# Performance work log

Hardware: AMD Instinct MI355X
Metric: run time of the kernel (lower is better)

The kernel has to match this reference:

```python
import jax, jax.numpy as jnp
import numpy as np

B, N, D, H, DH = 2, 2048, 1024, 16, 64
SCALE = DH ** -0.5


def rotate_half(t):
    t1, t2 = jnp.split(t, 2, axis=-1)
    return jnp.concatenate([-t2, t1], axis=-1)


def setup_inputs() -> dict:
    key = jax.random.key(0)
    ks = jax.random.split(key, 10)
    x = jax.random.normal(ks[0], (B, N, D), jnp.float32)
    mask = jnp.ones((B, N), bool)
    rotary_emb = jax.random.normal(ks[1], (N, DH), jnp.float32)
    attn_bias = jax.random.normal(ks[2], (H, N, N), jnp.float32)
    value_residual = jax.random.normal(ks[3], (B, H, N, DH), jnp.float32)
    s = D ** -0.5
    Wq = jax.random.normal(ks[4], (D, H * DH), jnp.float32) * s
    Wkv = jax.random.normal(ks[5], (D, 2 * H * DH), jnp.float32) * s
    Wmix = jax.random.normal(ks[6], (D, H), jnp.float32) * s
    Wout = jax.random.normal(ks[7], (H * DH, D), jnp.float32) * s
    bout = jnp.zeros((D,), jnp.float32)
    return {"x": x, "mask": mask, "rotary_emb": rotary_emb, "attn_bias": attn_bias,
            "value_residual": value_residual, "Wq": Wq, "Wkv": Wkv, "Wmix": Wmix,
            "Wout": Wout, "bout": bout}


def reference(x, mask, rotary_emb, attn_bias, value_residual, Wq, Wkv, Wmix, Wout, bout):
    b, n, _ = x.shape
    # QKV projections (self-attention: context = x)
    q = (x @ Wq).reshape(b, n, H, DH).transpose(0, 2, 1, 3)          # b h n d
    kv = (x @ Wkv).reshape(b, n, 2, H, DH).transpose(2, 0, 3, 1, 4)
    k, v = kv[0], kv[1]                                              # b h n d each
    # value-residual lerp: v.lerp(residual, mix) = v + mix*(residual - v)
    mix = jax.nn.sigmoid(x @ Wmix).transpose(0, 2, 1)[..., None]     # b h n 1
    v = v + mix * (value_residual - v)
    # rotary position embedding on q and k
    cos = jnp.cos(rotary_emb)[None, None]                            # 1 1 n d
    sin = jnp.sin(rotary_emb)[None, None]
    q = q * cos + rotate_half(q) * sin
    k = k * cos + rotate_half(k) * sin
    # scaled dot-product attention with bias and key-padding mask
    sim = jnp.einsum('bhid,bhjd->bhij', q, k) * SCALE + attn_bias[None]
    neg = jnp.finfo(sim.dtype).min
    sim = jnp.where(mask[:, None, None, :], sim, neg)
    attn = jax.nn.softmax(sim, axis=-1)
    out = jnp.einsum('bhij,bhjd->bhid', attn, v)
    out = out.transpose(0, 2, 1, 3).reshape(b, n, H * DH)
    return out @ Wout + bout
```

## Files before the change

kernel.cpp:

```cpp
#include <hip/hip_runtime.h>
#include <hip/hip_bf16.h>
#include <cstdint>
#include <cstddef>

#define B_    2
#define N_    2048
#define D_    1024
#define H_    16
#define DH_   64
#define HD_   1024
#define QKVW_ 3072
#define SCALE_ 0.125f

typedef unsigned short ushort_t;
typedef __attribute__((ext_vector_type(8))) short bf16x8;
typedef __attribute__((ext_vector_type(4))) float f32x4;
typedef _Float16 f16_t;
typedef __attribute__((ext_vector_type(8))) _Float16 f16x8;

__device__ __forceinline__ float bfb(unsigned v) {
  union { unsigned u; float f; } c; c.u = v << 16; return c.f;
}
__device__ __forceinline__ float bf2f(ushort_t v) { return bfb((unsigned)v); }
__device__ __forceinline__ ushort_t f2bf(float f) {
  unsigned u = __float_as_uint(f);
  return (ushort_t)((u + 0x7fffu + ((u >> 16) & 1u)) >> 16);
}
__device__ __forceinline__ ushort_t f2h_bits(float f) {
  union { f16_t h; ushort_t u; } c; c.h = (f16_t)f; return c.u;
}

template<bool F32>
__device__ __forceinline__ float ld1(const void* p, size_t i) {
  if (F32) return ((const float*)p)[i];
  else     return bf2f(((const ushort_t*)p)[i]);
}
template<bool F32>
__device__ __forceinline__ void ld4(const void* p, size_t i, float* o) {
  if (F32) {
    float4 v = *(const float4*)((const float*)p + i);
    o[0] = v.x; o[1] = v.y; o[2] = v.z; o[3] = v.w;
  } else {
    ushort4 v = *(const ushort4*)((const ushort_t*)p + i);
    o[0] = bf2f(v.x); o[1] = bf2f(v.y); o[2] = bf2f(v.z); o[3] = bf2f(v.w);
  }
}

__global__ __launch_bounds__(256) void detect_kernel(const unsigned* __restrict__ xbits,
                                                     int* __restrict__ flag) {
  __shared__ int cnt[256];
  int tid = threadIdx.x, bad = 0;
  for (int i = tid; i < 4096; i += 256) {
    unsigned w = xbits[i];
    bad += (((w >> 7) & 0xffu) >= 0xF0u) + (((w >> 23) & 0xffu) >= 0xF0u);
  }
  cnt[tid] = bad;
  __syncthreads();
  for (int s = 128; s > 0; s >>= 1) {
    if (tid < s) cnt[tid] += cnt[tid + s];
    __syncthreads();
  }
  if (tid == 0) *flag = (cnt[0] > 4) ? 1 : 0;
}

template<bool F32>
__global__ __launch_bounds__(64) void mix_kernel(const int* __restrict__ flag,
                                                 const void* __restrict__ x,
                                                 const void* __restrict__ Wmix,
                                                 float* __restrict__ mix) {
  if ((*flag == 1) != F32) return;
  int row  = blockIdx.x;
  int lane = threadIdx.x;
  int h = lane >> 2, part = lane & 3;
  float acc = 0.f;
  int kbase = part * 256;
  for (int t = 0; t < 256; ++t) {
    int k = kbase + t;
    acc = fmaf(ld1<F32>(x, (size_t)row * D_ + k), ld1<F32>(Wmix, (size_t)k * H_ + h), acc);
  }
  acc += __shfl_xor(acc, 1);
  acc += __shfl_xor(acc, 2);
  if (part == 0) mix[(size_t)row * H_ + h] = 1.f / (1.f + __expf(-acc));
}

template<bool F32>
__global__ __launch_bounds__(256) void gemm_qkv_mfma(const int* __restrict__ flag,
                                                     const void* __restrict__ X,
                                                     const void* __restrict__ Wq,
                                                     const void* __restrict__ Wkv,
                                                     ushort_t* __restrict__ C) {
  if ((*flag == 1) != F32) return;
  __shared__ ushort_t As[128 * 40];
  __shared__ ushort_t Bs[128 * 40];
  int tid  = threadIdx.x;
  int w    = tid >> 6, lane = tid & 63;
  int ln   = lane & 15, quad = lane >> 4;
  int wr   = w >> 1, wc = w & 1;
  int n0   = blockIdx.x * 128, m0 = blockIdx.y * 128;
  const void* Bp; int ldb, nb;
  if (n0 < 1024) { Bp = Wq;  ldb = 1024; nb = n0; }
  else           { Bp = Wkv; ldb = 2048; nb = n0 - 1024; }

  f32x4 acc[4][4] = {};

  for (int kt = 0; kt < 32; ++kt) {
    int k0 = kt * 32;
#pragma unroll
    for (int i = 0; i < 2; ++i) {
      int f   = tid + 256 * i;
      int row = f >> 2, c8 = (f & 3) << 3;
      float at[8];
      ld4<F32>(X, (size_t)(m0 + row) * D_ + k0 + c8,     at);
      ld4<F32>(X, (size_t)(m0 + row) * D_ + k0 + c8 + 4, at + 4);
      union { ushort_t s[8]; uint4 u; } hh;
#pragma unroll
      for (int j = 0; j < 8; ++j) hh.s[j] = f2h_bits(at[j]);
      *(uint4*)&As[row * 40 + c8] = hh.u;
    }
#pragma unroll
    for (int i = 0; i < 2; ++i) {
      int p  = tid + 256 * i;
      int kp = p >> 5, c4 = (p & 31) << 2;
      float b0[4], b1[4];
      ld4<F32>(Bp, (size_t)(k0 + 2 * kp)     * ldb + nb + c4, b0);
      ld4<F32>(Bp, (size_t)(k0 + 2 * kp + 1) * ldb + nb + c4, b1);
#pragma unroll
      for (int j = 0; j < 4; ++j) {
        int n  = c4 + j;
        int kk = (2 * kp) ^ (((n >> 2) & 7) << 2);
        *(unsigned*)&Bs[n * 40 + kk] =
            (unsigned)f2h_bits(b0[j]) | ((unsigned)f2h_bits(b1[j]) << 16);
      }
    }
    __syncthreads();
    f16x8 af[4];
#pragma unroll
    for (int i = 0; i < 4; ++i)
      af[i] = *(const f16x8*)&As[(wr * 64 + i * 16 + ln) * 40 + quad * 8];
#pragma unroll
    for (int jb = 0; jb < 4; ++jb) {
      int n = wc * 64 + jb * 16 + ln;
      int ps = ((n >> 2) & 7) << 2;
      union { ushort4 q[2]; f16x8 v; } bf;
      bf.q[0] = *(const ushort4*)&Bs[n * 40 + ((quad * 8)     ^ ps)];
      bf.q[1] = *(const ushort4*)&Bs[n * 40 + ((quad * 8 + 4) ^ ps)];
#pragma unroll
      for (int i = 0; i < 4; ++i)
        acc[i][jb] = __builtin_amdgcn_mfma_f32_16x16x32_f16(af[i], bf.v, acc[i][jb], 0, 0, 0);
    }
    __syncthreads();
  }
#pragma unroll
  for (int i = 0; i < 4; ++i) {
    int row = m0 + wr * 64 + i * 16 + quad * 4;
#pragma unroll
    for (int jb = 0; jb < 4; ++jb) {
      int col = n0 + wc * 64 + jb * 16 + ln;
#pragma unroll
      for (int r = 0; r < 4; ++r)
        C[(size_t)(row + r) * QKVW_ + col] = f2bf(acc[i][jb][r]);
    }
  }
}

template<bool F32>
__global__ __launch_bounds__(256) void rotlerp(const int* __restrict__ flag,
                                               ushort_t* __restrict__ qkv,
                                               const void* __restrict__ rot,
                                               const float* __restrict__ mix,
                                               const void* __restrict__ resid) {
  if ((*flag == 1) != F32) return;
  int lane = threadIdx.x & 63;
  int row  = blockIdx.x * 4 + (threadIdx.x >> 6);
  int h  = row & 15;
  int bn = row >> 4;
  int n  = bn & (N_ - 1);
  int b  = bn >> 11;
  size_t base = (size_t)bn * QKVW_ + h * DH_;
  float q = bf2f(qkv[base + lane]);
  float k = bf2f(qkv[base + 1024 + lane]);
  float v = bf2f(qkv[base + 2048 + lane]);
  float ang = ld1<F32>(rot, (size_t)n * DH_ + lane);
  float sn, cs;
  __sincosf(ang, &sn, &cs);
  float qp = __shfl_xor(q, 32);
  float kp = __shfl_xor(k, 32);
  float sgn = (lane < 32) ? -1.f : 1.f;
  float qn = fmaf(q, cs, sgn * qp * sn);
  float kn = fmaf(k, cs, sgn * kp * sn);
  float m = mix[(size_t)bn * H_ + h];
  float r = ld1<F32>(resid, ((size_t)(b * H_ + h) * N_ + n) * DH_ + lane);
  float vn = fmaf(m, r - v, v);
  qkv[base + lane]        = f2bf(qn);
  qkv[base + 1024 + lane] = f2bf(kn);
  qkv[base + 2048 + lane] = f2bf(vn);
}

template<bool F32>
__global__ __launch_bounds__(256) void attn_mfma(const int* __restrict__ flag,
                                                 const ushort_t* __restrict__ qkv,
                                                 const void* __restrict__ bias,
                                                 ushort_t* __restrict__ obuf) {
  if ((*flag == 1) != F32) return;
  __shared__ ushort_t Ks[64 * 72];
  __shared__ ushort_t Vt[64 * 72];
  __shared__ ushort_t Ps[4][16 * 72];
  int tid  = threadIdx.x;
  int w    = tid >> 6, lane = tid & 63;
  int ln   = lane & 15, quad = lane >> 4;
  int q0   = blockIdx.x * 64, h = blockIdx.y, b = blockIdx.z;

  bf16x8 aq0, aq1;
  {
    const ushort_t* qp = qkv + (size_t)(b * N_ + q0 + 16 * w + ln) * QKVW_ + h * DH_ + quad * 8;
    union { uint4 u; bf16x8 v; } c0, c1;
    c0.u = *(const uint4*)qp;
    c1.u = *(const uint4*)(qp + 32);
    aq0 = c0.v; aq1 = c1.v;
  }
  bf16x8 one_b;
  {
    union { ushort_t s[8]; bf16x8 v; } ob;
#pragma unroll
    for (int i = 0; i < 8; ++i) ob.s[i] = (ln == 0) ? (ushort_t)0x3F80 : (ushort_t)0;
    one_b = ob.v;
  }

  f32x4 o[5] = {};
  float mrow[4] = {-1e30f, -1e30f, -1e30f, -1e30f};

  int rA = tid >> 3;
  int cc = tid & 7;
  int dd = cc * 8;
  uint4 kA, kB, vA, vB;
  float bbA[4][4], bbB[4][4];

  auto loadKV = [&](int t) {
    int j0 = t * 64;
    const ushort_t* kp = qkv + (size_t)(b * N_ + j0 + rA) * QKVW_ + 1024 + h * DH_ + dd;
    kA = *(const uint4*)kp;
    vA = *(const uint4*)(kp + 1024);
    kB = *(const uint4*)(kp + (size_t)32 * QKVW_);
    vB = *(const uint4*)(kp + (size_t)32 * QKVW_ + 1024);
  };
  auto writeKV = [&]() {
    *(uint4*)&Ks[rA * 72 + dd]        = kA;
    *(uint4*)&Ks[(rA + 32) * 72 + dd] = kB;
    union { uint4 u; ushort_t s[8]; } ua, ub;
    ua.u = vA; ub.u = vB;
    int colA = (rA + 8 * cc) & 63;
    int colB = (rA + 32 + 8 * cc) & 63;
#pragma unroll
    for (int i = 0; i < 8; ++i) {
      Vt[(dd + i) * 72 + colA] = ua.s[i];
      Vt[(dd + i) * 72 + colB] = ub.s[i];
    }
  };
  auto loadBias = [&](int t, float (&bb)[4][4]) {
    int j0 = t * 64;
    size_t rbase = (size_t)h * N_ + q0 + 16 * w + quad * 4;
#pragma unroll
    for (int r = 0; r < 4; ++r)
#pragma unroll
      for (int c = 0; c < 4; ++c)
        bb[r][c] = ld1<F32>(bias, (rbase + r) * N_ + j0 + 16 * c + ln);
  };
  auto tileCompute = [&](const float (&bb)[4][4]) {
    f32x4 s[4] = {};
#pragma unroll
    for (int jb = 0; jb < 4; ++jb) {
      bf16x8 k0 = *(const bf16x8*)&Ks[(jb * 16 + ln) * 72 + quad * 8];
      bf16x8 k1 = *(const bf16x8*)&Ks[(jb * 16 + ln) * 72 + 32 + quad * 8];
      s[jb] = __builtin_amdgcn_mfma_f32_16x16x32_bf16(aq0, k0, s[jb], 0, 0, 0);
      s[jb] = __builtin_amdgcn_mfma_f32_16x16x32_bf16(aq1, k1, s[jb], 0, 0, 0);
    }
    float vv[4][4], tm[4];
    float g = -1e30f;
#pragma unroll
    for (int r = 0; r < 4; ++r) {
#pragma unroll
      for (int c = 0; c < 4; ++c) vv[r][c] = fmaf(s[c][r], SCALE_, bb[r][c]);
      float t01 = fmaxf(vv[r][0], vv[r][1]);
      float t23 = fmaxf(vv[r][2], vv[r][3]);
      float tmx = fmaxf(t01, t23);
      tmx = fmaxf(tmx, __shfl_xor(tmx, 1));
      tmx = fmaxf(tmx, __shfl_xor(tmx, 2));
      tmx = fmaxf(tmx, __shfl_xor(tmx, 4));
      tmx = fmaxf(tmx, __shfl_xor(tmx, 8));
      tm[r] = tmx;
      g = fmaxf(g, tmx - mrow[r]);
    }
    if (!__all(g <= 8.f)) {
#pragma unroll
      for (int r = 0; r < 4; ++r) {
        float mnew = fmaxf(mrow[r], tm[r]);
        float al = __expf(mrow[r] - mnew);
        mrow[r] = mnew;
#pragma unroll
        for (int d5 = 0; d5 < 5; ++d5) o[d5][r] *= al;
      }
    }
#pragma unroll
    for (int r = 0; r < 4; ++r) {
#pragma unroll
      for (int c = 0; c < 4; ++c) {
        float p = __expf(vv[r][c] - mrow[r]);
        Ps[w][(quad * 4 + r) * 72 + c * 16 + ln] = f2bf(p);
      }
    }
    bf16x8 ap0 = *(const bf16x8*)&Ps[w][ln * 72 + quad * 8];
    bf16x8 ap1 = *(const bf16x8*)&Ps[w][ln * 72 + 32 + quad * 8];
#pragma unroll
    for (int db = 0; db < 4; ++db) {
      int row = db * 16 + ln;
      int rot = (quad * 8 + 8 * (2 * db + (ln >> 3))) & 63;
      bf16x8 v0 = *(const bf16x8*)&Vt[row * 72 + rot];
      bf16x8 v1 = *(const bf16x8*)&Vt[row * 72 + ((rot + 32) & 63)];
      o[db] = __builtin_amdgcn_mfma_f32_16x16x32_bf16(ap0, v0, o[db], 0, 0, 0);
      o[db] = __builtin_amdgcn_mfma_f32_16x16x32_bf16(ap1, v1, o[db], 0, 0, 0);
    }
    o[4] = __builtin_amdgcn_mfma_f32_16x16x32_bf16(ap0, one_b, o[4], 0, 0, 0);
    o[4] = __builtin_amdgcn_mfma_f32_16x16x32_bf16(ap1, one_b, o[4], 0, 0, 0);
  };

  loadKV(0);
  loadBias(0, bbA);
  writeKV();
  __syncthreads();

  for (int t = 0; t < 32; t += 2) {
    loadKV(t + 1);
    loadBias(t + 1, bbB);
    tileCompute(bbA);
    __syncthreads();
    writeKV();
    __syncthreads();
    if (t + 2 < 32) { loadKV(t + 2); loadBias(t + 2, bbA); }
    tileCompute(bbB);
    if (t + 2 < 32) {
      __syncthreads();
      writeKV();
      __syncthreads();
    }
  }

#pragma unroll
  for (int r = 0; r < 4; ++r) {
    float ls  = __shfl(o[4][r], lane & 48);
    float inv = 1.f / ls;
    ushort_t* op = obuf + (size_t)(b * N_ + q0 + 16 * w + quad * 4 + r) * HD_ + h * DH_;
#pragma unroll
    for (int db = 0; db < 4; ++db) op[db * 16 + ln] = f2bf(o[db][r] * inv);
  }
}

template<bool F32>
__global__ __launch_bounds__(256) void gemm_out_mfma(const int* __restrict__ flag,
                                                     const ushort_t* __restrict__ A,
                                                     const void* __restrict__ W,
                                                     const void* __restrict__ bvec,
                                                     void* __restrict__ C) {
  if ((*flag == 1) != F32) return;
  __shared__ ushort_t As[128 * 40];
  __shared__ ushort_t Bs[64 * 40];
  int tid  = threadIdx.x;
  int w    = tid >> 6, lane = tid & 63;
  int ln   = lane & 15, quad = lane >> 4;
  int wr   = w >> 1, wc = w & 1;
  int n0   = blockIdx.x * 64, m0 = blockIdx.y * 128;

  f32x4 acc[4][2] = {};

  for (int kt = 0; kt < 32; ++kt) {
    int k0 = kt * 32;
#pragma unroll
    for (int i = 0; i < 2; ++i) {
      int f   = tid + 256 * i;
      int row = f >> 2, c8 = (f & 3) << 3;
      const ushort_t* ap = A + (size_t)(m0 + row) * HD_ + k0 + c8;
      ushort4 u0 = *(const ushort4*)ap;
      ushort4 u1 = *(const ushort4*)(ap + 4);
      union { ushort_t s[8]; uint4 u; } hh;
      hh.s[0] = f2h_bits(bf2f(u0.x)); hh.s[1] = f2h_bits(bf2f(u0.y));
      hh.s[2] = f2h_bits(bf2f(u0.z)); hh.s[3] = f2h_bits(bf2f(u0.w));
      hh.s[4] = f2h_bits(bf2f(u1.x)); hh.s[5] = f2h_bits(bf2f(u1.y));
      hh.s[6] = f2h_bits(bf2f(u1.z)); hh.s[7] = f2h_bits(bf2f(u1.w));
      *(uint4*)&As[row * 40 + c8] = hh.u;
    }
    {
      int kp = tid >> 4, c4 = (tid & 15) << 2;
      float b0[4], b1[4];
      ld4<F32>(W, (size_t)(k0 + 2 * kp)     * HD_ + n0 + c4, b0);
      ld4<F32>(W, (size_t)(k0 + 2 * kp + 1) * HD_ + n0 + c4, b1);
#pragma unroll
      for (int j = 0; j < 4; ++j) {
        int n  = c4 + j;
        int kk = (2 * kp) ^ (((n >> 2) & 7) << 2);
        *(unsigned*)&Bs[n * 40 + kk] =
            (unsigned)f2h_bits(b0[j]) | ((unsigned)f2h_bits(b1[j]) << 16);
      }
    }
    __syncthreads();
    f16x8 af[4];
#pragma unroll
    for (int i = 0; i < 4; ++i)
      af[i] = *(const f16x8*)&As[(wr * 64 + i * 16 + ln) * 40 + quad * 8];
#pragma unroll
    for (int jb = 0; jb < 2; ++jb) {
      int n = wc * 32 + jb * 16 + ln;
      int ps = ((n >> 2) & 7) << 2;
      union { ushort4 q[2]; f16x8 v; } bf;
      bf.q[0] = *(const ushort4*)&Bs[n * 40 + ((quad * 8)     ^ ps)];
      bf.q[1] = *(const ushort4*)&Bs[n * 40 + ((quad * 8 + 4) ^ ps)];
#pragma unroll
      for (int i = 0; i < 4; ++i)
        acc[i][jb] = __builtin_amdgcn_mfma_f32_16x16x32_f16(af[i], bf.v, acc[i][jb], 0, 0, 0);
    }
    __syncthreads();
  }
#pragma unroll
  for (int i = 0; i < 4; ++i) {
    int row = m0 + wr * 64 + i * 16 + quad * 4;
#pragma unroll
    for (int jb = 0; jb < 2; ++jb) {
      int col = n0 + wc * 32 + jb * 16 + ln;
      float bv = ld1<F32>(bvec, col);
#pragma unroll
      for (int r = 0; r < 4; ++r) {
        float rv = acc[i][jb][r] + bv;
        size_t idx = (size_t)(row + r) * HD_ + col;
        if (F32) ((float*)C)[idx] = rv;
        else     ((ushort_t*)C)[idx] = f2bf(rv);
      }
    }
  }
}

extern "C" void kernel_launch(void* const* d_in, const int* in_sizes, int n_in,
                              void* d_out, int out_size, void* d_ws, size_t ws_size,
                              hipStream_t stream) {
  const void* x     = d_in[0];
  const void* rot   = d_in[2];
  const void* bias  = d_in[3];
  const void* resid = d_in[4];
  const void* Wq    = d_in[5];
  const void* Wkv   = d_in[6];
  const void* Wmix  = d_in[7];
  const void* Wout  = d_in[8];
  const void* bout  = d_in[9];

  int*      dflag  = (int*)d_ws;
  float*    mixbuf = (float*)((char*)d_ws + 256);
  ushort_t* qkv    = (ushort_t*)((char*)d_ws + 256 + (size_t)B_ * N_ * H_ * sizeof(float));
  ushort_t* obuf   = qkv + (size_t)B_ * N_ * QKVW_;

  detect_kernel<<<1, 256, 0, stream>>>((const unsigned*)x, dflag);

  mix_kernel<false><<<B_ * N_, 64, 0, stream>>>(dflag, x, Wmix, mixbuf);
  mix_kernel<true ><<<B_ * N_, 64, 0, stream>>>(dflag, x, Wmix, mixbuf);

  dim3 gq(QKVW_ / 128, (B_ * N_) / 128);
  gemm_qkv_mfma<false><<<gq, 256, 0, stream>>>(dflag, x, Wq, Wkv, qkv);
  gemm_qkv_mfma<true ><<<gq, 256, 0, stream>>>(dflag, x, Wq, Wkv, qkv);

  rotlerp<false><<<(B_ * N_ * H_) / 4, 256, 0, stream>>>(dflag, qkv, rot, mixbuf, resid);
  rotlerp<true ><<<(B_ * N_ * H_) / 4, 256, 0, stream>>>(dflag, qkv, rot, mixbuf, resid);

  dim3 ga(N_ / 64, H_, B_);
  attn_mfma<false><<<ga, 256, 0, stream>>>(dflag, qkv, bias, obuf);
  attn_mfma<true ><<<ga, 256, 0, stream>>>(dflag, qkv, bias, obuf);

  dim3 go(HD_ / 64, (B_ * N_) / 128);
  gemm_out_mfma<false><<<go, 256, 0, stream>>>(dflag, obuf, Wout, bout, d_out);
  gemm_out_mfma<true ><<<go, 256, 0, stream>>>(dflag, obuf, Wout, bout, d_out);
}
```

Before: 659.0 us.

## Double attention block to 128 queries with 8 waves sharing K/V tiles

The attention kernel now runs 512 threads per block covering 128 query rows, so each K/V tile loaded into shared memory serves twice as many queries. Each thread loads one K/V row instead of two. The P staging buffer reuses the Ks region for half the waves, guarded by an added barrier after QK^T. The row max reduction switches from shuffles to DPP row operations, and s_setprio is raised around the MFMA sections. The risk is the extra barrier per tile, which must also keep the Ks aliasing from racing with the next tile's K writes.

```diff
diff --git a/kernel.cpp b/kernel.cpp
--- a/kernel.cpp
+++ b/kernel.cpp
@@ -28,6 +28,19 @@
 }
 __device__ __forceinline__ ushort_t f2h_bits(float f) {
   union { f16_t h; ushort_t u; } c; c.h = (f16_t)f; return c.u;
+}
+
+__device__ __forceinline__ float qmax16(float x) {
+  int t;
+  t = __builtin_amdgcn_mov_dpp(__float_as_int(x), 0x121, 0xf, 0xf, true);
+  x = fmaxf(x, __int_as_float(t));
+  t = __builtin_amdgcn_mov_dpp(__float_as_int(x), 0x122, 0xf, 0xf, true);
+  x = fmaxf(x, __int_as_float(t));
+  t = __builtin_amdgcn_mov_dpp(__float_as_int(x), 0x124, 0xf, 0xf, true);
+  x = fmaxf(x, __int_as_float(t));
+  t = __builtin_amdgcn_mov_dpp(__float_as_int(x), 0x128, 0xf, 0xf, true);
+  x = fmaxf(x, __int_as_float(t));
+  return x;
 }
 
 template<bool F32>
@@ -197,18 +210,18 @@
 }
 
 template<bool F32>
-__global__ __launch_bounds__(256) void attn_mfma(const int* __restrict__ flag,
-                                                 const ushort_t* __restrict__ qkv,
-                                                 const void* __restrict__ bias,
-                                                 ushort_t* __restrict__ obuf) {
+__global__ __launch_bounds__(512, 4) void attn_mfma(const int* __restrict__ flag,
+                                                    const ushort_t* __restrict__ qkv,
+                                                    const void* __restrict__ bias,
+                                                    ushort_t* __restrict__ obuf) {
   if ((*flag == 1) != F32) return;
   __shared__ ushort_t Ks[64 * 72];
   __shared__ ushort_t Vt[64 * 72];
-  __shared__ ushort_t Ps[4][16 * 72];
+  __shared__ ushort_t Pex[64 * 72];
   int tid  = threadIdx.x;
   int w    = tid >> 6, lane = tid & 63;
   int ln   = lane & 15, quad = lane >> 4;
-  int q0   = blockIdx.x * 64, h = blockIdx.y, b = blockIdx.z;
+  int q0   = blockIdx.x * 128, h = blockIdx.y, b = blockIdx.z;
 
   bf16x8 aq0, aq1;
   {
@@ -225,6 +238,7 @@
     for (int i = 0; i < 8; ++i) ob.s[i] = (ln == 0) ? (ushort_t)0x3F80 : (ushort_t)0;
     one_b = ob.v;
   }
+  ushort_t* psB = (w < 4) ? &Ks[(16 * w) * 72] : &Pex[(16 * (w - 4)) * 72];
 
   f32x4 o[5] = {};
   float mrow[4] = {-1e30f, -1e30f, -1e30f, -1e30f};
@@ -232,41 +246,33 @@
   int rA = tid >> 3;
   int cc = tid & 7;
   int dd = cc * 8;
-  uint4 kA, kB, vA, vB;
+  uint4 kA, vA;
   float bbA[4][4], bbB[4][4];
 
   auto loadKV = [&](int t) {
-    int j0 = t * 64;
-    const ushort_t* kp = qkv + (size_t)(b * N_ + j0 + rA) * QKVW_ + 1024 + h * DH_ + dd;
+    const ushort_t* kp = qkv + (size_t)(b * N_ + t * 64 + rA) * QKVW_ + 1024 + h * DH_ + dd;
     kA = *(const uint4*)kp;
     vA = *(const uint4*)(kp + 1024);
-    kB = *(const uint4*)(kp + (size_t)32 * QKVW_);
-    vB = *(const uint4*)(kp + (size_t)32 * QKVW_ + 1024);
   };
   auto writeKV = [&]() {
-    *(uint4*)&Ks[rA * 72 + dd]        = kA;
-    *(uint4*)&Ks[(rA + 32) * 72 + dd] = kB;
-    union { uint4 u; ushort_t s[8]; } ua, ub;
-    ua.u = vA; ub.u = vB;
-    int colA = (rA + 8 * cc) & 63;
-    int colB = (rA + 32 + 8 * cc) & 63;
-#pragma unroll
-    for (int i = 0; i < 8; ++i) {
-      Vt[(dd + i) * 72 + colA] = ua.s[i];
-      Vt[(dd + i) * 72 + colB] = ub.s[i];
-    }
+    *(uint4*)&Ks[rA * 72 + dd] = kA;
+    union { uint4 u; ushort_t s[8]; } ua;
+    ua.u = vA;
+    int colA = (rA + dd) & 63;
+#pragma unroll
+    for (int i = 0; i < 8; ++i) Vt[(dd + i) * 72 + colA] = ua.s[i];
   };
   auto loadBias = [&](int t, float (&bb)[4][4]) {
-    int j0 = t * 64;
     size_t rbase = (size_t)h * N_ + q0 + 16 * w + quad * 4;
 #pragma unroll
     for (int r = 0; r < 4; ++r)
 #pragma unroll
       for (int c = 0; c < 4; ++c)
-        bb[r][c] = ld1<F32>(bias, (rbase + r) * N_ + j0 + 16 * c + ln);
+        bb[r][c] = ld1<F32>(bias, (rbase + r) * N_ + t * 64 + 16 * c + ln);
   };
   auto tileCompute = [&](const float (&bb)[4][4]) {
     f32x4 s[4] = {};
+    __builtin_amdgcn_s_setprio(1);
 #pragma unroll
     for (int jb = 0; jb < 4; ++jb) {
       bf16x8 k0 = *(const bf16x8*)&Ks[(jb * 16 + ln) * 72 + quad * 8];
@@ -274,6 +280,8 @@
       s[jb] = __builtin_amdgcn_mfma_f32_16x16x32_bf16(aq0, k0, s[jb], 0, 0, 0);
       s[jb] = __builtin_amdgcn_mfma_f32_16x16x32_bf16(aq1, k1, s[jb], 0, 0, 0);
     }
+    __builtin_amdgcn_s_setprio(0);
+    __syncthreads();
     float vv[4][4], tm[4];
     float g = -1e30f;
 #pragma unroll
@@ -282,13 +290,8 @@
       for (int c = 0; c < 4; ++c) vv[r][c] = fmaf(s[c][r], SCALE_, bb[r][c]);
       float t01 = fmaxf(vv[r][0], vv[r][1]);
       float t23 = fmaxf(vv[r][2], vv[r][3]);
-      float tmx = fmaxf(t01, t23);
-      tmx = fmaxf(tmx, __shfl_xor(tmx, 1));
-      tmx = fmaxf(tmx, __shfl_xor(tmx, 2));
-      tmx = fmaxf(tmx, __shfl_xor(tmx, 4));
-      tmx = fmaxf(tmx, __shfl_xor(tmx, 8));
-      tm[r] = tmx;
-      g = fmaxf(g, tmx - mrow[r]);
+      tm[r] = qmax16(fmaxf(t01, t23));
+      g = fmaxf(g, tm[r] - mrow[r]);
     }
     if (!__all(g <= 8.f)) {
 #pragma unroll
@@ -305,11 +308,12 @@
 #pragma unroll
       for (int c = 0; c < 4; ++c) {
         float p = __expf(vv[r][c] - mrow[r]);
-        Ps[w][(quad * 4 + r) * 72 + c * 16 + ln] = f2bf(p);
+        psB[(quad * 4 + r) * 72 + c * 16 + ln] = f2bf(p);
       }
     }
-    bf16x8 ap0 = *(const bf16x8*)&Ps[w][ln * 72 + quad * 8];
-    bf16x8 ap1 = *(const bf16x8*)&Ps[w][ln * 72 + 32 + quad * 8];
+    bf16x8 ap0 = *(const bf16x8*)&psB[ln * 72 + quad * 8];
+    bf16x8 ap1 = *(const bf16x8*)&psB[ln * 72 + 32 + quad * 8];
+    __builtin_amdgcn_s_setprio(1);
 #pragma unroll
     for (int db = 0; db < 4; ++db) {
       int row = db * 16 + ln;
@@ -321,6 +325,7 @@
     }
     o[4] = __builtin_amdgcn_mfma_f32_16x16x32_bf16(ap0, one_b, o[4], 0, 0, 0);
     o[4] = __builtin_amdgcn_mfma_f32_16x16x32_bf16(ap1, one_b, o[4], 0, 0, 0);
+    __builtin_amdgcn_s_setprio(0);
   };
 
   loadKV(0);
@@ -466,9 +471,9 @@
   rotlerp<false><<<(B_ * N_ * H_) / 4, 256, 0, stream>>>(dflag, qkv, rot, mixbuf, resid);
   rotlerp<true ><<<(B_ * N_ * H_) / 4, 256, 0, stream>>>(dflag, qkv, rot, mixbuf, resid);
 
-  dim3 ga(N_ / 64, H_, B_);
-  attn_mfma<false><<<ga, 256, 0, stream>>>(dflag, qkv, bias, obuf);
-  attn_mfma<true ><<<ga, 256, 0, stream>>>(dflag, qkv, bias, obuf);
+  dim3 ga(N_ / 128, H_, B_);
+  attn_mfma<false><<<ga, 512, 0, stream>>>(dflag, qkv, bias, obuf);
+  attn_mfma<true ><<<ga, 512, 0, stream>>>(dflag, qkv, bias, obuf);
 
   dim3 go(HD_ / 64, (B_ * N_) / 128);
   gemm_out_mfma<false><<<go, 256, 0, stream>>>(dflag, obuf, Wout, bout, d_out);
```

Result: faster. 621.7 us (-5.6%).
